# Performance work log

Hardware: AMD Instinct MI355X
Metric: run time of the kernel (lower is better)

## Reference

```python
import jax, jax.numpy as jnp
import numpy as np

D_MODEL = 512
SEQ_LEN = 2048
S = 32  # local window size
BATCH = 2


def setup_inputs() -> dict:
    key = jax.random.key(0)
    ks = jax.random.split(key, 12)
    shp = (SEQ_LEN, BATCH, D_MODEL)
    return {
        "query": jax.random.normal(ks[0], shp, jnp.float32),
        "key": jax.random.normal(ks[1], shp, jnp.float32),
        "value": jax.random.normal(ks[2], shp, jnp.float32),
        "Wq": jax.random.normal(ks[3], (D_MODEL, D_MODEL), jnp.float32) * 0.02,
        "bq": jax.random.normal(ks[4], (D_MODEL,), jnp.float32) * 0.01,
        "Wk": jax.random.normal(ks[5], (D_MODEL, D_MODEL), jnp.float32) * 0.02,
        "bk": jax.random.normal(ks[6], (D_MODEL,), jnp.float32) * 0.01,
        "Wv": jax.random.normal(ks[7], (D_MODEL, D_MODEL), jnp.float32) * 0.02,
        "bv": jax.random.normal(ks[8], (D_MODEL,), jnp.float32) * 0.01,
        "pos_bias": jax.random.normal(ks[9], (SEQ_LEN, SEQ_LEN), jnp.float32) * 0.02,
        "Wo": jax.random.normal(ks[10], (D_MODEL, D_MODEL), jnp.float32) * 0.02,
        "bo": jax.random.normal(ks[11], (D_MODEL,), jnp.float32) * 0.01,
    }


def _aft_local(query, key, value, Wq, bq, Wk, bk, Wv, bv, pos_bias, Wo, bo):
    T, B, D = query.shape
    q = query @ Wq.T + bq  # [T,B,D]
    k = key @ Wk.T + bk
    v = value @ Wv.T + bv
    pb = pos_bias[:T, :T]

    # max_logit: elementwise max of per-dim key max and (key + col-max of pos_bias) max,
    # then batch index 0 (faithful to original `[0]` indexing) -> shape [D]
    max_logit = jnp.maximum(k.max(axis=0),
                            (k + pb.max(axis=0)[:, None, None]).max(axis=0))[0]

    # out-of-window running sums: tokens t' <= t - S contribute exp(k) (no pos bias)
    ek = jnp.exp(k - max_logit)                 # [T,B,D]
    cs_num = jnp.cumsum(ek * v, axis=0)
    cs_den = jnp.cumsum(ek, axis=0)
    t_arr = jnp.arange(T)
    prefix_idx = jnp.clip(t_arr - S, 0, T - 1)
    has_prefix = (t_arr >= S)[:, None, None]
    num_out = jnp.where(has_prefix, cs_num[prefix_idx], 0.0)
    den_out = jnp.where(has_prefix, cs_den[prefix_idx], 0.0)

    # in-window part: t' in [max(0, t-S+1), t] with pos_bias[t, t']
    j = jnp.arange(S)
    idx_raw = t_arr[:, None] - S + 1 + j[None, :]   # [T,S]
    valid = (idx_raw >= 0).astype(k.dtype)
    idx = jnp.clip(idx_raw, 0, T - 1)
    k_win = k[idx]                                  # [T,S,B,D]
    v_win = v[idx]                                  # [T,S,B,D]
    pb_win = pb[t_arr[:, None], idx]                # [T,S]
    exp_l = jnp.exp(k_win + pb_win[:, :, None, None] - max_logit) * valid[:, :, None, None]
    num_in = (exp_l * v_win).sum(axis=1)            # [T,B,D]
    den_in = exp_l.sum(axis=1)

    y = jax.nn.sigmoid(q) * (num_out + num_in) / (den_out + den_in)
    return y @ Wo.T + bo


def reference(query, key, value, Wq, bq, Wk, bk, Wv, bv, pos_bias, Wo, bo):
    return _aft_local(query, key, value, Wq, bq, Wk, bk, Wv, bv, pos_bias, Wo, bo)
```

## Files before the change

kernel.cpp:

```cpp
#include <hip/hip_runtime.h>
#include <hip/hip_bf16.h>

#define TT 2048
#define BB 2
#define DD 512
#define BD (BB*DD)
#define SS 32
#define MR (TT*BB)
#define NE (TT*BB*DD)
#define CH 32

typedef __bf16 bf16x8 __attribute__((ext_vector_type(8)));
typedef float f32x4 __attribute__((ext_vector_type(4)));

__device__ __forceinline__ void async_copy16(void* lds, const void* gptr) {
    __builtin_amdgcn_global_load_lds(
        (const __attribute__((address_space(1))) void*)gptr,
        (__attribute__((address_space(3))) void*)lds,
        16, 0, 0);
}

__global__ __launch_bounds__(256) void gemm_bf16_nt_bias(
    const __hip_bfloat16* __restrict__ A0, const __hip_bfloat16* __restrict__ A1,
    const __hip_bfloat16* __restrict__ A2,
    const __hip_bfloat16* __restrict__ W0, const __hip_bfloat16* __restrict__ W1,
    const __hip_bfloat16* __restrict__ W2,
    const float* __restrict__ b0, const float* __restrict__ b1,
    const float* __restrict__ b2,
    float* __restrict__ C0, float* __restrict__ C1, float* __restrict__ C2)
{
    const int z = blockIdx.z;
    const __hip_bfloat16* A = z == 0 ? A0 : (z == 1 ? A1 : A2);
    const __hip_bfloat16* W = z == 0 ? W0 : (z == 1 ? W1 : W2);
    const float* bias       = z == 0 ? b0 : (z == 1 ? b1 : b2);
    float* C                = z == 0 ? C0 : (z == 1 ? C1 : C2);
    const int K = DD, N = DD;

    __shared__ char smem[8192];
    const int tid = threadIdx.x;
    const int lane = tid & 63;
    const int wv = tid >> 6;
    const int wave_m = wv >> 1;
    const int wave_n = wv & 1;
    const int m0 = blockIdx.y * 64;
    const int n0 = blockIdx.x * 64;

    f32x4 acc[2][2] = {};

    const __hip_bfloat16* Arow = A + (size_t)(m0 + lane) * K + wv * 8;
    const __hip_bfloat16* Wrow = W + (size_t)(n0 + lane) * K + wv * 8;
    char* ldsA = &smem[wv * 1024];
    char* ldsW = &smem[4096 + wv * 1024];

    const int kq = lane >> 4;
    const int rr = lane & 15;

    for (int k0 = 0; k0 < K; k0 += 32) {
        __syncthreads();
        async_copy16(ldsA, Arow + k0);
        async_copy16(ldsW, Wrow + k0);
        __syncthreads();

        bf16x8 a0 = *(const bf16x8*)&smem[kq*1024 + (wave_m*32 +  0 + rr)*16];
        bf16x8 a1 = *(const bf16x8*)&smem[kq*1024 + (wave_m*32 + 16 + rr)*16];
        bf16x8 b0v = *(const bf16x8*)&smem[4096 + kq*1024 + (wave_n*32 +  0 + rr)*16];
        bf16x8 b1v = *(const bf16x8*)&smem[4096 + kq*1024 + (wave_n*32 + 16 + rr)*16];

        acc[0][0] = __builtin_amdgcn_mfma_f32_16x16x32_bf16(a0, b0v, acc[0][0], 0, 0, 0);
        acc[0][1] = __builtin_amdgcn_mfma_f32_16x16x32_bf16(a0, b1v, acc[0][1], 0, 0, 0);
        acc[1][0] = __builtin_amdgcn_mfma_f32_16x16x32_bf16(a1, b0v, acc[1][0], 0, 0, 0);
        acc[1][1] = __builtin_amdgcn_mfma_f32_16x16x32_bf16(a1, b1v, acc[1][1], 0, 0, 0);
    }

    #pragma unroll
    for (int ms = 0; ms < 2; ++ms) {
        #pragma unroll
        for (int ns = 0; ns < 2; ++ns) {
            int n = n0 + wave_n*32 + ns*16 + rr;
            float bn = bias[n];
            #pragma unroll
            for (int r = 0; r < 4; ++r) {
                int m = m0 + wave_m*32 + ms*16 + kq*4 + r;
                C[(size_t)m * N + n] = acc[ms][ns][r] + bn;
            }
        }
    }
}

__global__ __launch_bounds__(256) void cast_all(
    const float* __restrict__ s0, const float* __restrict__ s1, const float* __restrict__ s2,
    const float* __restrict__ w0, const float* __restrict__ w1,
    const float* __restrict__ w2, const float* __restrict__ w3,
    __hip_bfloat16* __restrict__ d0, __hip_bfloat16* __restrict__ d1, __hip_bfloat16* __restrict__ d2,
    __hip_bfloat16* __restrict__ e0, __hip_bfloat16* __restrict__ e1,
    __hip_bfloat16* __restrict__ e2, __hip_bfloat16* __restrict__ e3)
{
    int b = blockIdx.x;
    const float* s;
    __hip_bfloat16* d;
    size_t i;
    if (b < 6144) {
        int which = b >> 11;
        s = which == 0 ? s0 : (which == 1 ? s1 : s2);
        d = which == 0 ? d0 : (which == 1 ? d1 : d2);
        i = ((size_t)(b & 2047) * 256 + threadIdx.x) * 4;
    } else {
        int b2 = b - 6144;
        int which = b2 >> 8;
        s = which == 0 ? w0 : (which == 1 ? w1 : (which == 2 ? w2 : w3));
        d = which == 0 ? e0 : (which == 1 ? e1 : (which == 2 ? e2 : e3));
        i = ((size_t)(b2 & 255) * 256 + threadIdx.x) * 4;
    }
    float4 f = *(const float4*)(s + i);
    union { __hip_bfloat16 h[4]; ushort4 u; } cv;
    cv.h[0] = __float2bfloat16(f.x); cv.h[1] = __float2bfloat16(f.y);
    cv.h[2] = __float2bfloat16(f.z); cv.h[3] = __float2bfloat16(f.w);
    *(ushort4*)((unsigned short*)d + i) = cv.u;
}

__global__ __launch_bounds__(256) void partials_kernel(
    const float* __restrict__ kk, const float* __restrict__ vv,
    float* __restrict__ part_d, float* __restrict__ part_n)
{
    int col = blockIdx.x * 256 + threadIdx.x;
    int chunk = blockIdx.y;
    float sd = 0.f, sn = 0.f;
    int t0 = chunk * CH;
    for (int t = t0; t < t0 + CH; ++t) {
        size_t off = (size_t)t * BD + col;
        float e = expf(kk[off]);
        sd += e;
        sn += e * vv[off];
    }
    part_d[(size_t)chunk * BD + col] = sd;
    part_n[(size_t)chunk * BD + col] = sn;
}

__global__ __launch_bounds__(256) void fused_window(
    const float* __restrict__ q, const float* __restrict__ kk,
    const float* __restrict__ vv, const float* __restrict__ part_d,
    const float* __restrict__ part_n, const float* __restrict__ pb,
    __hip_bfloat16* __restrict__ yb)
{
    __shared__ float wl[CH][SS];
    const int tid = threadIdx.x;
    const int col = blockIdx.x * 256 + tid;
    const int chunk = blockIdx.y;
    const int t0 = chunk * CH;

    #pragma unroll
    for (int i = 0; i < (CH * SS) / 256; ++i) {
        int idx = tid + i * 256;
        int tl = idx >> 5, j = idx & 31;
        int t = t0 + tl;
        int u = t - (SS - 1) + j;
        float w = 0.f;
        if (u >= 0) w = expf(pb[(size_t)t * TT + u]);
        wl[tl][j] = w;
    }
    __syncthreads();

    float ring_d[32], ring_n[32];
    float cs_d = 0.f, cs_n = 0.f;
    const bool hasp = (chunk > 0);
    if (hasp) {
        float pref_d = 0.f, pref_n = 0.f;
        for (int p = 0; p < chunk; ++p) {
            pref_d += part_d[(size_t)p * BD + col];
            pref_n += part_n[(size_t)p * BD + col];
        }
        float ssd = 0.f, ssn = 0.f;
        #pragma unroll
        for (int i = 0; i < 32; ++i) {
            size_t off = (size_t)(t0 - 32 + i) * BD + col;
            float e = expf(kk[off]);
            float n = e * vv[off];
            ring_d[i] = e; ring_n[i] = n;
            ssd += e; ssn += n;
        }
        cs_d = pref_d - ssd;
        cs_n = pref_n - ssn;
    } else {
        #pragma unroll
        for (int i = 0; i < 32; ++i) { ring_d[i] = 0.f; ring_n[i] = 0.f; }
    }

    #pragma unroll
    for (int s = 0; s < CH; ++s) {
        int t = t0 + s;
        size_t off = (size_t)t * BD + col;
        float e = expf(kk[off]);
        float n = e * vv[off];
        cs_d += ring_d[s];
        cs_n += ring_n[s];
        ring_d[s] = e;
        ring_n[s] = n;
        float den = 0.f, num = 0.f;
        #pragma unroll
        for (int j4 = 0; j4 < 8; ++j4) {
            float4 w4 = *(const float4*)&wl[s][j4 * 4];
            den += w4.x * ring_d[(s + 1 + j4*4 + 0) & 31];
            num += w4.x * ring_n[(s + 1 + j4*4 + 0) & 31];
            den += w4.y * ring_d[(s + 1 + j4*4 + 1) & 31];
            num += w4.y * ring_n[(s + 1 + j4*4 + 1) & 31];
            den += w4.z * ring_d[(s + 1 + j4*4 + 2) & 31];
            num += w4.z * ring_n[(s + 1 + j4*4 + 2) & 31];
            den += w4.w * ring_d[(s + 1 + j4*4 + 3) & 31];
            num += w4.w * ring_n[(s + 1 + j4*4 + 3) & 31];
        }
        if (hasp) { den += cs_d; num += cs_n; }
        float qv = q[off];
        float sig = 1.f / (1.f + expf(-qv));
        yb[off] = __float2bfloat16(sig * num / den);
    }
}

extern "C" void kernel_launch(void* const* d_in, const int* in_sizes, int n_in,
                              void* d_out, int out_size, void* d_ws, size_t ws_size,
                              hipStream_t stream) {
    const float* query = (const float*)d_in[0];
    const float* key   = (const float*)d_in[1];
    const float* value = (const float*)d_in[2];
    const float* Wq    = (const float*)d_in[3];
    const float* bq    = (const float*)d_in[4];
    const float* Wk    = (const float*)d_in[5];
    const float* bk    = (const float*)d_in[6];
    const float* Wv    = (const float*)d_in[7];
    const float* bv    = (const float*)d_in[8];
    const float* pb    = (const float*)d_in[9];
    const float* Wo    = (const float*)d_in[10];
    const float* bo    = (const float*)d_in[11];
    float* out = (float*)d_out;

    float* ws = (float*)d_ws;
    float* q      = ws;
    float* kk     = ws + (size_t)NE;
    float* vv     = ws + (size_t)2 * NE;
    float* part_d = ws + (size_t)3 * NE;
    float* part_n = part_d + 65536;
    __hip_bfloat16* bfb = (__hip_bfloat16*)(part_n + 65536);
    __hip_bfloat16* qb  = bfb;
    __hip_bfloat16* kb  = bfb + (size_t)NE;
    __hip_bfloat16* vb  = bfb + (size_t)2 * NE;
    __hip_bfloat16* yb  = bfb + (size_t)3 * NE;
    __hip_bfloat16* Wqb = bfb + (size_t)4 * NE;
    __hip_bfloat16* Wkb = Wqb + 262144;
    __hip_bfloat16* Wvb = Wkb + 262144;
    __hip_bfloat16* Wob = Wvb + 262144;

    cast_all<<<7168, 256, 0, stream>>>(query, key, value, Wq, Wk, Wv, Wo,
                                       qb, kb, vb, Wqb, Wkb, Wvb, Wob);

    dim3 gemm_grid(DD / 64, MR / 64, 3);
    gemm_bf16_nt_bias<<<gemm_grid, 256, 0, stream>>>(
        qb, kb, vb, Wqb, Wkb, Wvb, bq, bk, bv, q, kk, vv);

    partials_kernel<<<dim3(BD / 256, TT / CH), 256, 0, stream>>>(kk, vv, part_d, part_n);

    fused_window<<<dim3(BD / 256, TT / CH), 256, 0, stream>>>(
        q, kk, vv, part_d, part_n, pb, yb);

    dim3 gemm_grid1(DD / 64, MR / 64, 1);
    gemm_bf16_nt_bias<<<gemm_grid1, 256, 0, stream>>>(
        yb, yb, yb, Wob, Wob, Wob, bo, bo, bo, out, out, out);
}
```

Before: 182.6 us.

## Fuse bf16 casts into GEMMs and move exp/partial sums into QKV epilogue

The separate cast kernel is removed: the GEMMs now load fp32 inputs and weights and convert them to bf16 while staging into LDS. The K and V projections share one block, and the epilogue computes exp(k) and exp(k)*v, stores them, and reduces the per-chunk partial sums through shuffles and LDS. This removes the partials kernel and the exp work in the window kernel. The cost is that weights are reconverted in every block and staging uses synchronous loads instead of async LDS copies, and the K/V block carries more accumulator registers.

```diff
diff --git a/kernel.cpp b/kernel.cpp
--- a/kernel.cpp
+++ b/kernel.cpp
@@ -20,125 +20,149 @@
         16, 0, 0);
 }
 
-__global__ __launch_bounds__(256) void gemm_bf16_nt_bias(
-    const __hip_bfloat16* __restrict__ A0, const __hip_bfloat16* __restrict__ A1,
-    const __hip_bfloat16* __restrict__ A2,
-    const __hip_bfloat16* __restrict__ W0, const __hip_bfloat16* __restrict__ W1,
-    const __hip_bfloat16* __restrict__ W2,
-    const float* __restrict__ b0, const float* __restrict__ b1,
-    const float* __restrict__ b2,
-    float* __restrict__ C0, float* __restrict__ C1, float* __restrict__ C2)
+__device__ __forceinline__ void stage_cvt(
+    const float* __restrict__ src, int row0, int k0,
+    char* lds, int row, int kq)
 {
-    const int z = blockIdx.z;
-    const __hip_bfloat16* A = z == 0 ? A0 : (z == 1 ? A1 : A2);
-    const __hip_bfloat16* W = z == 0 ? W0 : (z == 1 ? W1 : W2);
-    const float* bias       = z == 0 ? b0 : (z == 1 ? b1 : b2);
-    float* C                = z == 0 ? C0 : (z == 1 ? C1 : C2);
-    const int K = DD, N = DD;
-
-    __shared__ char smem[8192];
+    const float* p = src + (size_t)(row0 + row) * DD + k0 + kq * 8;
+    float4 f0 = *(const float4*)p;
+    float4 f1 = *(const float4*)(p + 4);
+    union { __hip_bfloat16 h[8]; int4 v; } u;
+    u.h[0] = __float2bfloat16(f0.x); u.h[1] = __float2bfloat16(f0.y);
+    u.h[2] = __float2bfloat16(f0.z); u.h[3] = __float2bfloat16(f0.w);
+    u.h[4] = __float2bfloat16(f1.x); u.h[5] = __float2bfloat16(f1.y);
+    u.h[6] = __float2bfloat16(f1.z); u.h[7] = __float2bfloat16(f1.w);
+    *(int4*)(lds + kq * 1024 + row * 16) = u.v;
+}
+
+__global__ __launch_bounds__(256) void gemm_qkv(
+    const float* __restrict__ query, const float* __restrict__ key,
+    const float* __restrict__ value,
+    const float* __restrict__ Wq, const float* __restrict__ Wk,
+    const float* __restrict__ Wv,
+    const float* __restrict__ bq, const float* __restrict__ bk,
+    const float* __restrict__ bv,
+    float* __restrict__ qout, float* __restrict__ ek, float* __restrict__ ekv,
+    float* __restrict__ part_d, float* __restrict__ part_n)
+{
+    __shared__ char smem[16384];
     const int tid = threadIdx.x;
     const int lane = tid & 63;
     const int wv = tid >> 6;
-    const int wave_m = wv >> 1;
-    const int wave_n = wv & 1;
-    const int m0 = blockIdx.y * 64;
-    const int n0 = blockIdx.x * 64;
-
-    f32x4 acc[2][2] = {};
-
-    const __hip_bfloat16* Arow = A + (size_t)(m0 + lane) * K + wv * 8;
-    const __hip_bfloat16* Wrow = W + (size_t)(n0 + lane) * K + wv * 8;
-    char* ldsA = &smem[wv * 1024];
-    char* ldsW = &smem[4096 + wv * 1024];
-
-    const int kq = lane >> 4;
-    const int rr = lane & 15;
-
-    for (int k0 = 0; k0 < K; k0 += 32) {
+    const int wave_m = wv >> 1, wave_n = wv & 1;
+    const int m0 = blockIdx.y * 64, n0 = blockIdx.x * 64;
+    const int kq = lane >> 4, rr = lane & 15;
+    const int srow = tid & 63, skq = tid >> 6;
+
+    if (blockIdx.z == 0) {
+        f32x4 acc[2][2] = {};
+        for (int k0 = 0; k0 < DD; k0 += 32) {
+            __syncthreads();
+            stage_cvt(query, m0, k0, smem, srow, skq);
+            stage_cvt(Wq, n0, k0, smem + 4096, srow, skq);
+            __syncthreads();
+            bf16x8 a0 = *(const bf16x8*)&smem[kq*1024 + (wave_m*32 +  0 + rr)*16];
+            bf16x8 a1 = *(const bf16x8*)&smem[kq*1024 + (wave_m*32 + 16 + rr)*16];
+            bf16x8 b0 = *(const bf16x8*)&smem[4096 + kq*1024 + (wave_n*32 +  0 + rr)*16];
+            bf16x8 b1 = *(const bf16x8*)&smem[4096 + kq*1024 + (wave_n*32 + 16 + rr)*16];
+            acc[0][0] = __builtin_amdgcn_mfma_f32_16x16x32_bf16(a0, b0, acc[0][0], 0, 0, 0);
+            acc[0][1] = __builtin_amdgcn_mfma_f32_16x16x32_bf16(a0, b1, acc[0][1], 0, 0, 0);
+            acc[1][0] = __builtin_amdgcn_mfma_f32_16x16x32_bf16(a1, b0, acc[1][0], 0, 0, 0);
+            acc[1][1] = __builtin_amdgcn_mfma_f32_16x16x32_bf16(a1, b1, acc[1][1], 0, 0, 0);
+        }
+        #pragma unroll
+        for (int ms = 0; ms < 2; ++ms)
+            #pragma unroll
+            for (int ns = 0; ns < 2; ++ns) {
+                int n = n0 + wave_n*32 + ns*16 + rr;
+                float bn = bq[n];
+                #pragma unroll
+                for (int r = 0; r < 4; ++r) {
+                    int m = m0 + wave_m*32 + ms*16 + kq*4 + r;
+                    qout[(size_t)m * DD + n] = acc[ms][ns][r] + bn;
+                }
+            }
+    } else {
+        f32x4 acck[2][2] = {}, accv[2][2] = {};
+        for (int k0 = 0; k0 < DD; k0 += 32) {
+            __syncthreads();
+            stage_cvt(key,   m0, k0, smem,         srow, skq);
+            stage_cvt(Wk,    n0, k0, smem + 4096,  srow, skq);
+            stage_cvt(value, m0, k0, smem + 8192,  srow, skq);
+            stage_cvt(Wv,    n0, k0, smem + 12288, srow, skq);
+            __syncthreads();
+            bf16x8 ak0 = *(const bf16x8*)&smem[kq*1024 + (wave_m*32 +  0 + rr)*16];
+            bf16x8 ak1 = *(const bf16x8*)&smem[kq*1024 + (wave_m*32 + 16 + rr)*16];
+            bf16x8 bk0 = *(const bf16x8*)&smem[4096 + kq*1024 + (wave_n*32 +  0 + rr)*16];
+            bf16x8 bk1 = *(const bf16x8*)&smem[4096 + kq*1024 + (wave_n*32 + 16 + rr)*16];
+            bf16x8 av0 = *(const bf16x8*)&smem[8192 + kq*1024 + (wave_m*32 +  0 + rr)*16];
+            bf16x8 av1 = *(const bf16x8*)&smem[8192 + kq*1024 + (wave_m*32 + 16 + rr)*16];
+            bf16x8 bv0 = *(const bf16x8*)&smem[12288 + kq*1024 + (wave_n*32 +  0 + rr)*16];
+            bf16x8 bv1 = *(const bf16x8*)&smem[12288 + kq*1024 + (wave_n*32 + 16 + rr)*16];
+            acck[0][0] = __builtin_amdgcn_mfma_f32_16x16x32_bf16(ak0, bk0, acck[0][0], 0, 0, 0);
+            acck[0][1] = __builtin_amdgcn_mfma_f32_16x16x32_bf16(ak0, bk1, acck[0][1], 0, 0, 0);
+            acck[1][0] = __builtin_amdgcn_mfma_f32_16x16x32_bf16(ak1, bk0, acck[1][0], 0, 0, 0);
+            acck[1][1] = __builtin_amdgcn_mfma_f32_16x16x32_bf16(ak1, bk1, acck[1][1], 0, 0, 0);
+            accv[0][0] = __builtin_amdgcn_mfma_f32_16x16x32_bf16(av0, bv0, accv[0][0], 0, 0, 0);
+            accv[0][1] = __builtin_amdgcn_mfma_f32_16x16x32_bf16(av0, bv1, accv[0][1], 0, 0, 0);
+            accv[1][0] = __builtin_amdgcn_mfma_f32_16x16x32_bf16(av1, bv0, accv[1][0], 0, 0, 0);
+            accv[1][1] = __builtin_amdgcn_mfma_f32_16x16x32_bf16(av1, bv1, accv[1][1], 0, 0, 0);
+        }
+        float sd[2][2] = {{0.f,0.f},{0.f,0.f}};
+        float sn[2][2] = {{0.f,0.f},{0.f,0.f}};
+        #pragma unroll
+        for (int ms = 0; ms < 2; ++ms)
+            #pragma unroll
+            for (int ns = 0; ns < 2; ++ns) {
+                int n = n0 + wave_n*32 + ns*16 + rr;
+                float bkn = bk[n], bvn = bv[n];
+                #pragma unroll
+                for (int r = 0; r < 4; ++r) {
+                    int m = m0 + wave_m*32 + ms*16 + kq*4 + r;
+                    float e  = expf(acck[ms][ns][r] + bkn);
+                    float nv = e * (accv[ms][ns][r] + bvn);
+                    ek[(size_t)m * DD + n]  = e;
+                    ekv[(size_t)m * DD + n] = nv;
+                    sd[ns][r & 1] += e;
+                    sn[ns][r & 1] += nv;
+                }
+            }
+        #pragma unroll
+        for (int ns = 0; ns < 2; ++ns)
+            #pragma unroll
+            for (int par = 0; par < 2; ++par) {
+                sd[ns][par] += __shfl_xor(sd[ns][par], 16, 64);
+                sd[ns][par] += __shfl_xor(sd[ns][par], 32, 64);
+                sn[ns][par] += __shfl_xor(sn[ns][par], 16, 64);
+                sn[ns][par] += __shfl_xor(sn[ns][par], 32, 64);
+            }
         __syncthreads();
-        async_copy16(ldsA, Arow + k0);
-        async_copy16(ldsW, Wrow + k0);
+        float* red = (float*)smem;
+        if (lane < 16) {
+            #pragma unroll
+            for (int ns = 0; ns < 2; ++ns) {
+                int c = wave_n*32 + ns*16 + rr;
+                red[(0*2 + wave_m)*64 + c] = sd[ns][0];
+                red[(1*2 + wave_m)*64 + c] = sd[ns][1];
+                red[(2*2 + wave_m)*64 + c] = sn[ns][0];
+                red[(3*2 + wave_m)*64 + c] = sn[ns][1];
+            }
+        }
         __syncthreads();
-
-        bf16x8 a0 = *(const bf16x8*)&smem[kq*1024 + (wave_m*32 +  0 + rr)*16];
-        bf16x8 a1 = *(const bf16x8*)&smem[kq*1024 + (wave_m*32 + 16 + rr)*16];
-        bf16x8 b0v = *(const bf16x8*)&smem[4096 + kq*1024 + (wave_n*32 +  0 + rr)*16];
-        bf16x8 b1v = *(const bf16x8*)&smem[4096 + kq*1024 + (wave_n*32 + 16 + rr)*16];
-
-        acc[0][0] = __builtin_amdgcn_mfma_f32_16x16x32_bf16(a0, b0v, acc[0][0], 0, 0, 0);
-        acc[0][1] = __builtin_amdgcn_mfma_f32_16x16x32_bf16(a0, b1v, acc[0][1], 0, 0, 0);
-        acc[1][0] = __builtin_amdgcn_mfma_f32_16x16x32_bf16(a1, b0v, acc[1][0], 0, 0, 0);
-        acc[1][1] = __builtin_amdgcn_mfma_f32_16x16x32_bf16(a1, b1v, acc[1][1], 0, 0, 0);
-    }
-
-    #pragma unroll
-    for (int ms = 0; ms < 2; ++ms) {
-        #pragma unroll
-        for (int ns = 0; ns < 2; ++ns) {
-            int n = n0 + wave_n*32 + ns*16 + rr;
-            float bn = bias[n];
-            #pragma unroll
-            for (int r = 0; r < 4; ++r) {
-                int m = m0 + wave_m*32 + ms*16 + kq*4 + r;
-                C[(size_t)m * N + n] = acc[ms][ns][r] + bn;
-            }
-        }
-    }
-}
-
-__global__ __launch_bounds__(256) void cast_all(
-    const float* __restrict__ s0, const float* __restrict__ s1, const float* __restrict__ s2,
-    const float* __restrict__ w0, const float* __restrict__ w1,
-    const float* __restrict__ w2, const float* __restrict__ w3,
-    __hip_bfloat16* __restrict__ d0, __hip_bfloat16* __restrict__ d1, __hip_bfloat16* __restrict__ d2,
-    __hip_bfloat16* __restrict__ e0, __hip_bfloat16* __restrict__ e1,
-    __hip_bfloat16* __restrict__ e2, __hip_bfloat16* __restrict__ e3)
-{
-    int b = blockIdx.x;
-    const float* s;
-    __hip_bfloat16* d;
-    size_t i;
-    if (b < 6144) {
-        int which = b >> 11;
-        s = which == 0 ? s0 : (which == 1 ? s1 : s2);
-        d = which == 0 ? d0 : (which == 1 ? d1 : d2);
-        i = ((size_t)(b & 2047) * 256 + threadIdx.x) * 4;
-    } else {
-        int b2 = b - 6144;
-        int which = b2 >> 8;
-        s = which == 0 ? w0 : (which == 1 ? w1 : (which == 2 ? w2 : w3));
-        d = which == 0 ? e0 : (which == 1 ? e1 : (which == 2 ? e2 : e3));
-        i = ((size_t)(b2 & 255) * 256 + threadIdx.x) * 4;
-    }
-    float4 f = *(const float4*)(s + i);
-    union { __hip_bfloat16 h[4]; ushort4 u; } cv;
-    cv.h[0] = __float2bfloat16(f.x); cv.h[1] = __float2bfloat16(f.y);
-    cv.h[2] = __float2bfloat16(f.z); cv.h[3] = __float2bfloat16(f.w);
-    *(ushort4*)((unsigned short*)d + i) = cv.u;
-}
-
-__global__ __launch_bounds__(256) void partials_kernel(
-    const float* __restrict__ kk, const float* __restrict__ vv,
-    float* __restrict__ part_d, float* __restrict__ part_n)
-{
-    int col = blockIdx.x * 256 + threadIdx.x;
-    int chunk = blockIdx.y;
-    float sd = 0.f, sn = 0.f;
-    int t0 = chunk * CH;
-    for (int t = t0; t < t0 + CH; ++t) {
-        size_t off = (size_t)t * BD + col;
-        float e = expf(kk[off]);
-        sd += e;
-        sn += e * vv[off];
-    }
-    part_d[(size_t)chunk * BD + col] = sd;
-    part_n[(size_t)chunk * BD + col] = sn;
+        {
+            int which = tid >> 6;
+            int c = tid & 63;
+            float s = red[(which*2 + 0)*64 + c] + red[(which*2 + 1)*64 + c];
+            int b = which & 1;
+            float* dst = (which < 2) ? part_d : part_n;
+            dst[(size_t)blockIdx.y * BD + b*512 + n0 + c] = s;
+        }
+    }
 }
 
 __global__ __launch_bounds__(256) void fused_window(
-    const float* __restrict__ q, const float* __restrict__ kk,
-    const float* __restrict__ vv, const float* __restrict__ part_d,
+    const float* __restrict__ q, const float* __restrict__ ek,
+    const float* __restrict__ ekv, const float* __restrict__ part_d,
     const float* __restrict__ part_n, const float* __restrict__ pb,
     __hip_bfloat16* __restrict__ yb)
 {
@@ -173,8 +197,8 @@
         #pragma unroll
         for (int i = 0; i < 32; ++i) {
             size_t off = (size_t)(t0 - 32 + i) * BD + col;
-            float e = expf(kk[off]);
-            float n = e * vv[off];
+            float e = ek[off];
+            float n = ekv[off];
             ring_d[i] = e; ring_n[i] = n;
             ssd += e; ssn += n;
         }
@@ -189,8 +213,8 @@
     for (int s = 0; s < CH; ++s) {
         int t = t0 + s;
         size_t off = (size_t)t * BD + col;
-        float e = expf(kk[off]);
-        float n = e * vv[off];
+        float e = ek[off];
+        float n = ekv[off];
         cs_d += ring_d[s];
         cs_n += ring_n[s];
         ring_d[s] = e;
@@ -213,6 +237,51 @@
         float sig = 1.f / (1.f + expf(-qv));
         yb[off] = __float2bfloat16(sig * num / den);
     }
+}
+
+__global__ __launch_bounds__(256) void gemm_out(
+    const __hip_bfloat16* __restrict__ yb, const float* __restrict__ Wo,
+    const float* __restrict__ bo, float* __restrict__ out)
+{
+    __shared__ char smem[8192];
+    const int tid = threadIdx.x;
+    const int lane = tid & 63;
+    const int wv = tid >> 6;
+    const int wave_m = wv >> 1, wave_n = wv & 1;
+    const int m0 = blockIdx.y * 64, n0 = blockIdx.x * 64;
+    const int kq = lane >> 4, rr = lane & 15;
+    const int srow = tid & 63, skq = tid >> 6;
+
+    f32x4 acc[2][2] = {};
+    const __hip_bfloat16* Arow = yb + (size_t)(m0 + lane) * DD + wv * 8;
+    char* ldsA = &smem[wv * 1024];
+
+    for (int k0 = 0; k0 < DD; k0 += 32) {
+        __syncthreads();
+        async_copy16(ldsA, Arow + k0);
+        stage_cvt(Wo, n0, k0, smem + 4096, srow, skq);
+        __syncthreads();
+        bf16x8 a0 = *(const bf16x8*)&smem[kq*1024 + (wave_m*32 +  0 + rr)*16];
+        bf16x8 a1 = *(const bf16x8*)&smem[kq*1024 + (wave_m*32 + 16 + rr)*16];
+        bf16x8 b0 = *(const bf16x8*)&smem[4096 + kq*1024 + (wave_n*32 +  0 + rr)*16];
+        bf16x8 b1 = *(const bf16x8*)&smem[4096 + kq*1024 + (wave_n*32 + 16 + rr)*16];
+        acc[0][0] = __builtin_amdgcn_mfma_f32_16x16x32_bf16(a0, b0, acc[0][0], 0, 0, 0);
+        acc[0][1] = __builtin_amdgcn_mfma_f32_16x16x32_bf16(a0, b1, acc[0][1], 0, 0, 0);
+        acc[1][0] = __builtin_amdgcn_mfma_f32_16x16x32_bf16(a1, b0, acc[1][0], 0, 0, 0);
+        acc[1][1] = __builtin_amdgcn_mfma_f32_16x16x32_bf16(a1, b1, acc[1][1], 0, 0, 0);
+    }
+    #pragma unroll
+    for (int ms = 0; ms < 2; ++ms)
+        #pragma unroll
+        for (int ns = 0; ns < 2; ++ns) {
+            int n = n0 + wave_n*32 + ns*16 + rr;
+            float bn = bo[n];
+            #pragma unroll
+            for (int r = 0; r < 4; ++r) {
+                int m = m0 + wave_m*32 + ms*16 + kq*4 + r;
+                out[(size_t)m * DD + n] = acc[ms][ns][r] + bn;
+            }
+        }
 }
 
 extern "C" void kernel_launch(void* const* d_in, const int* in_sizes, int n_in,
@@ -234,33 +303,18 @@
 
     float* ws = (float*)d_ws;
     float* q      = ws;
-    float* kk     = ws + (size_t)NE;
-    float* vv     = ws + (size_t)2 * NE;
+    float* ek     = ws + (size_t)NE;
+    float* ekv    = ws + (size_t)2 * NE;
     float* part_d = ws + (size_t)3 * NE;
     float* part_n = part_d + 65536;
-    __hip_bfloat16* bfb = (__hip_bfloat16*)(part_n + 65536);
-    __hip_bfloat16* qb  = bfb;
-    __hip_bfloat16* kb  = bfb + (size_t)NE;
-    __hip_bfloat16* vb  = bfb + (size_t)2 * NE;
-    __hip_bfloat16* yb  = bfb + (size_t)3 * NE;
-    __hip_bfloat16* Wqb = bfb + (size_t)4 * NE;
-    __hip_bfloat16* Wkb = Wqb + 262144;
-    __hip_bfloat16* Wvb = Wkb + 262144;
-    __hip_bfloat16* Wob = Wvb + 262144;
-
-    cast_all<<<7168, 256, 0, stream>>>(query, key, value, Wq, Wk, Wv, Wo,
-                                       qb, kb, vb, Wqb, Wkb, Wvb, Wob);
-
-    dim3 gemm_grid(DD / 64, MR / 64, 3);
-    gemm_bf16_nt_bias<<<gemm_grid, 256, 0, stream>>>(
-        qb, kb, vb, Wqb, Wkb, Wvb, bq, bk, bv, q, kk, vv);
-
-    partials_kernel<<<dim3(BD / 256, TT / CH), 256, 0, stream>>>(kk, vv, part_d, part_n);
+    __hip_bfloat16* yb = (__hip_bfloat16*)(part_n + 65536);
+
+    gemm_qkv<<<dim3(DD / 64, MR / 64, 2), 256, 0, stream>>>(
+        query, key, value, Wq, Wk, Wv, bq, bk, bv,
+        q, ek, ekv, part_d, part_n);
 
     fused_window<<<dim3(BD / 256, TT / CH), 256, 0, stream>>>(
-        q, kk, vv, part_d, part_n, pb, yb);
-
-    dim3 gemm_grid1(DD / 64, MR / 64, 1);
-    gemm_bf16_nt_bias<<<gemm_grid1, 256, 0, stream>>>(
-        yb, yb, yb, Wob, Wob, Wob, bo, bo, bo, out, out, out);
-}
+        q, ek, ekv, part_d, part_n, pb, yb);
+
+    gemm_out<<<dim3(DD / 64, MR / 64), 256, 0, stream>>>(yb, Wo, bo, out);
+}
```

After: 204.2 us. 11.8% more time.
